# Optimization experiments

Measured on AMD Instinct MI355X. Metric: run time of the kernel, lower is better.

Reference implementation:

```python
import jax, jax.numpy as jnp
import numpy as np

H = 19  # input_size == hidden_size

def setup_inputs() -> dict:
    key = jax.random.key(0)
    ks = jax.random.split(key, 7)
    seq_len, batch = 2048, 1024
    s = 1.0 / np.sqrt(H)  # PyTorch default uniform(-1/sqrt(H), 1/sqrt(H))
    x = jax.random.normal(ks[0], (seq_len, batch, H), dtype=jnp.float32)
    W_ih = jax.random.uniform(ks[1], (3 * H, H), jnp.float32, -s, s)
    W_hh = jax.random.uniform(ks[2], (3 * H, H), jnp.float32, -s, s)
    b_ih = jax.random.uniform(ks[3], (3 * H,), jnp.float32, -s, s)
    b_hh = jax.random.uniform(ks[4], (3 * H,), jnp.float32, -s, s)
    W_out = jax.random.uniform(ks[5], (1, H), jnp.float32, -s, s)
    b_out = jax.random.uniform(ks[6], (1,), jnp.float32, -s, s)
    return {"x": x, "W_ih": W_ih, "W_hh": W_hh, "b_ih": b_ih,
            "b_hh": b_hh, "W_out": W_out, "b_out": b_out}

def _gru(x, W_ih, W_hh, b_ih, b_hh):
    # Precompute all input projections in one big GEMM: [T, B, 3H]
    xg = jnp.einsum('tbi,gi->tbg', x, W_ih) + b_ih
    Whr, Whz, Whn = W_hh[:H], W_hh[H:2*H], W_hh[2*H:]
    bhr, bhz, bhn = b_hh[:H], b_hh[H:2*H], b_hh[2*H:]
    h0 = jnp.zeros(x.shape[1:2] + (H,), dtype=x.dtype)

    def step(h, xg_t):
        xr, xz, xn = xg_t[:, :H], xg_t[:, H:2*H], xg_t[:, 2*H:]
        r = jax.nn.sigmoid(xr + h @ Whr.T + bhr)
        z = jax.nn.sigmoid(xz + h @ Whz.T + bhz)
        n = jnp.tanh(xn + r * (h @ Whn.T + bhn))
        h_new = (1.0 - z) * n + z * h
        return h_new, h_new

    _, r_out = jax.lax.scan(step, h0, xg)  # r_out: [T, B, H]
    return r_out

def reference(x, W_ih, W_hh, b_ih, b_hh, W_out, b_out):
    r_out = _gru(x, W_ih, W_hh, b_ih, b_hh)
    return r_out @ W_out.T + b_out  # [T, B, 1]
```

## Files before the change

kernel.cpp:

```cpp
#include <hip/hip_runtime.h>
#include <math.h>

#define HH 19
#define NG 57
#define SL 64
#define NB 1024
#define TT 2048

typedef float v2f __attribute__((ext_vector_type(2)));
typedef unsigned u2 __attribute__((ext_vector_type(2)));
typedef unsigned u32x4 __attribute__((ext_vector_type(4)));
typedef unsigned u32x2 __attribute__((ext_vector_type(2)));
typedef _Float16 v2h __attribute__((ext_vector_type(2)));

__device__ __forceinline__ float rlf(float v, int l) {
  return __uint_as_float(__builtin_amdgcn_readlane(__float_as_uint(v), l));
}
__device__ __forceinline__ float frcp(float v) { return __builtin_amdgcn_rcpf(v); }
__device__ __forceinline__ float fexp2(float v) {
#if __has_builtin(__builtin_amdgcn_exp2f)
  return __builtin_amdgcn_exp2f(v);
#else
  return exp2f(v);
#endif
}
__device__ __forceinline__ unsigned short f2h(float f) {
  return __builtin_bit_cast(unsigned short, (_Float16)f);
}
__device__ __forceinline__ float h2f(unsigned short u) {
  return (float)__builtin_bit_cast(_Float16, u);
}
__device__ __forceinline__ v2f mk2(float a, float b) { v2f r; r.x = a; r.y = b; return r; }
__device__ __forceinline__ v2f vfma(v2f a, v2f b, v2f c) {
#if __has_builtin(__builtin_elementwise_fma)
  return __builtin_elementwise_fma(a, b, c);
#else
  v2f r; r.x = fmaf(a.x, b.x, c.x); r.y = fmaf(a.y, b.y, c.y); return r;
#endif
}

#if __has_builtin(__builtin_amdgcn_fdot2)
__device__ __forceinline__ float dot2h(v2h w, unsigned d, float acc) {
  return __builtin_amdgcn_fdot2(w, __builtin_bit_cast(v2h, d), acc, false);
}
#else
__device__ __forceinline__ float dot2h(v2h w, unsigned d, float acc) {
  const float fl = h2f((unsigned short)(d & 0xffffu));
  const float fh = h2f((unsigned short)(d >> 16));
  return fmaf((float)w.x, fl, fmaf((float)w.y, fh, acc));
}
#endif

#if __has_builtin(__builtin_amdgcn_permlane32_swap)
#define HAVE_PLS 1
__device__ __forceinline__ u2 pls(float x) {
  unsigned u = __float_as_uint(x);
  return __builtin_amdgcn_permlane32_swap(u, u, false, false);
}
#else
#define HAVE_PLS 0
#endif

__global__ __launch_bounds__(256) void xg_proj4(
    const float* __restrict__ x, const float* __restrict__ Wih,
    const float* __restrict__ bih, const float* __restrict__ bhh,
    unsigned short* __restrict__ xg)
{
  __shared__ __align__(16) float ls[256 * 33];
  const int tid = threadIdx.x;
  const size_t pair0 = (size_t)blockIdx.x * 256;
  const float L2E = 1.4426950408889634f;

  {
    const float* __restrict__ src = x + pair0 * HH;
#pragma unroll
    for (int j = 0; j < HH; ++j) ls[j * 256 + tid] = src[j * 256 + tid];
  }
  __syncthreads();

  float xv[HH];
#pragma unroll
  for (int k = 0; k < HH; ++k) xv[k] = ls[tid * HH + k];
  __syncthreads();

  unsigned short* __restrict__ lsh = (unsigned short*)ls;
#pragma unroll 1
  for (int g = 0; g < NG; ++g) {
    float a = bih[g] + ((g < 2 * HH) ? bhh[g] : 0.0f);
#pragma unroll
    for (int k = 0; k < HH; ++k) a = fmaf(xv[k], Wih[g * HH + k], a);
    a *= (g < 2 * HH) ? -L2E : (2.0f * L2E);
    lsh[tid * 66 + g] = f2h(a);
  }
#pragma unroll
  for (int g = NG; g < SL; ++g) lsh[tid * 66 + g] = 0;
  __syncthreads();

  const unsigned* __restrict__ lsd = (const unsigned*)ls;
  unsigned* __restrict__ xgd = (unsigned*)xg;
#pragma unroll
  for (int i = 0; i < 32; ++i) {
    const int D = tid + i * 256;
    xgd[pair0 * 32 + D] = lsd[(D >> 5) * 33 + (D & 31)];
  }
}

__global__ void __launch_bounds__(64)
__attribute__((amdgpu_waves_per_eu(1, 1)))
gru_rec6(const unsigned short* __restrict__ xg, const float* __restrict__ Whh,
         const float* __restrict__ bhh, const float* __restrict__ Wout,
         const float* __restrict__ bout, float* __restrict__ out)
{
  __shared__ __align__(16) unsigned short hsh16[64];
  const int b = blockIdx.x;
  const int lane = threadIdx.x;
  const float L2E = 1.4426950408889634f;

  int row;
  if (lane < 32)      row = lane;
  else if (lane < 51) row = lane + 6;
  else if (lane < 57) row = lane - 19;
  else                row = 37;
  const bool isn = (row >= 2 * HH);
  const float s = isn ? (2.0f * L2E) : -L2E;

  v2h wh16[10], wo16[10];
#pragma unroll
  for (int j = 0; j < 10; ++j) {
    const int k0 = 2 * j, k1 = 2 * j + 1;
    wh16[j].x = (_Float16)(s * Whh[row * HH + k0]);
    wh16[j].y = (_Float16)((k1 < HH) ? s * Whh[row * HH + k1] : 0.0f);
    wo16[j].x = (_Float16)Wout[k0];
    wo16[j].y = (_Float16)((k1 < HH) ? Wout[k1] : 0.0f);
  }
  const float dinit = isn ? (2.0f * L2E * bhh[row]) : 0.0f;
  const float bo = bout[0];

  const int il = lane < HH ? lane : HH - 1;
  const int zaddr = ((il < 13) ? (19 + il) : (38 + il)) * 4;

#if HAVE_PLS
  bool loIsX;
  {
    unsigned l = (unsigned)lane;
    u2 pr = __builtin_amdgcn_permlane32_swap(l, l, false, false);
    loIsX = ((unsigned)__builtin_amdgcn_readlane((int)pr.x, 32) < 32u);
  }
#define LOBCAST(val, dst) do { u2 _s = pls(val);                        \
    dst = __uint_as_float(loIsX ? _s.x : _s.y); } while (0)
#define HIBCAST(val, dst) do { u2 _s = pls(val);                        \
    dst = __uint_as_float(loIsX ? _s.y : _s.x); } while (0)
#else
  const int loaddr = (lane & 31) * 4;
  const int hiaddr = ((lane & 31) | 32) * 4;
#define LOBCAST(val, dst) dst = __uint_as_float((unsigned)              \
    __builtin_amdgcn_ds_bpermute(loaddr, (int)__float_as_uint(val)))
#define HIBCAST(val, dst) dst = __uint_as_float((unsigned)              \
    __builtin_amdgcn_ds_bpermute(hiaddr, (int)__float_as_uint(val)))
#endif

  float h = 0.0f;

  const unsigned short* __restrict__ xb = xg + (size_t)b * SL + row;
#define LOADX(dst, trow) do { dst = xb[(size_t)(trow) * (NB * SL)]; } while (0)

  unsigned short s0, s1, s2, s3, s4, s5, s6, s7;
  LOADX(s0, 0); LOADX(s1, 1); LOADX(s2, 2); LOADX(s3, 3);
  LOADX(s4, 4); LOADX(s5, 5); LOADX(s6, 6); LOADX(s7, 7);

  u32x4 Pa = {0,0,0,0}, Ra = {0,0,0,0}, Pb, Rb;
  u32x2 Qa = {0,0}, Qb;

#define OPROJ16(Pi, Ri, Qi, ovar) do {                                  \
    float _o0 = bo, _o1 = 0.0f;                                         \
    _o0 = dot2h(wo16[0], Pi.x, _o0); _o1 = dot2h(wo16[1], Pi.y, _o1);   \
    _o0 = dot2h(wo16[2], Pi.z, _o0); _o1 = dot2h(wo16[3], Pi.w, _o1);   \
    _o0 = dot2h(wo16[4], Ri.x, _o0); _o1 = dot2h(wo16[5], Ri.y, _o1);   \
    _o0 = dot2h(wo16[6], Ri.z, _o0); _o1 = dot2h(wo16[7], Ri.w, _o1);   \
    _o0 = dot2h(wo16[8], Qi.x, _o0); _o1 = dot2h(wo16[9], Qi.y, _o1);   \
    ovar = _o0 + _o1;                                                   \
  } while (0)

#define BODY(tcur, slot, Pi, Ri, Qi, Po, Ro, Qo, ovar) do {             \
                       \
    float _a0 = dinit, _a1 = 0.0f;                                      \
    _a0 = dot2h(wh16[0], Pi.x, _a0); _a1 = dot2h(wh16[1], Pi.y, _a1);   \
    _a0 = dot2h(wh16[2], Pi.z, _a0); _a1 = dot2h(wh16[3], Pi.w, _a1);   \
    _a0 = dot2h(wh16[4], Ri.x, _a0); _a1 = dot2h(wh16[5], Ri.y, _a1);   \
    _a0 = dot2h(wh16[6], Ri.z, _a0); _a1 = dot2h(wh16[7], Ri.w, _a1);   \
    _a0 = dot2h(wh16[8], Qi.x, _a0); _a1 = dot2h(wh16[9], Qi.y, _a1);   \
    const float preh = _a0 + _a1;                                       \
    const float xv = h2f(slot);                                         \
    const float pre = xv + preh;                                        \
    const float sig = frcp(fexp2(pre) + 1.0f);                          \
    const int zzi = __builtin_amdgcn_ds_bpermute(                       \
        zaddr, (int)__float_as_uint(sig));                              \
    float rr; LOBCAST(sig, rr);                                         \
    const float arg = fmaf(rr, preh, xv);                               \
    const float nn = fmaf(-2.0f, frcp(fexp2(arg) + 1.0f), 1.0f);        \
    float nh; HIBCAST(nn, nh);                                          \
    const float zz = __uint_as_float((unsigned)zzi);                    \
    h = fmaf(zz, h - nh, nh);                                           \
    \
    hsh16[lane] = f2h(h);                                               \
    Po = *(const u32x4*)&hsh16[0];                                      \
    Ro = *(const u32x4*)&hsh16[8];                                      \
    Qo = *(const u32x2*)&hsh16[16];                                     \
          \
    OPROJ16(Pi, Ri, Qi, ovar);                                          \
    { const int _tl = ((tcur) + 8 < TT) ? (tcur) + 8 : TT - 1;          \
      LOADX(slot, _tl); }                                               \
  } while (0)

  float o0, o1, o2, o3, o4, o5, o6, o7;
  float* __restrict__ ob = out + b;

  for (int t = 0; t < TT; t += 8) {
    BODY(t + 0, s0, Pa, Ra, Qa, Pb, Rb, Qb, o0);
    BODY(t + 1, s1, Pb, Rb, Qb, Pa, Ra, Qa, o1);
    BODY(t + 2, s2, Pa, Ra, Qa, Pb, Rb, Qb, o2);
    BODY(t + 3, s3, Pb, Rb, Qb, Pa, Ra, Qa, o3);
    BODY(t + 4, s4, Pa, Ra, Qa, Pb, Rb, Qb, o4);
    BODY(t + 5, s5, Pb, Rb, Qb, Pa, Ra, Qa, o5);
    BODY(t + 6, s6, Pa, Ra, Qa, Pb, Rb, Qb, o6);
    BODY(t + 7, s7, Pb, Rb, Qb, Pa, Ra, Qa, o7);
    if (lane == 0) {
      ob[(size_t)((t > 0) ? t - 1 : 0) * NB] = o0;
      ob[(size_t)(t + 0) * NB] = o1;
      ob[(size_t)(t + 1) * NB] = o2;
      ob[(size_t)(t + 2) * NB] = o3;
      ob[(size_t)(t + 3) * NB] = o4;
      ob[(size_t)(t + 4) * NB] = o5;
      ob[(size_t)(t + 5) * NB] = o6;
      ob[(size_t)(t + 6) * NB] = o7;
    }
  }

  {
    float oe;
    OPROJ16(Pa, Ra, Qa, oe);
    if (lane == 0) ob[(size_t)(TT - 1) * NB] = oe;
  }

#undef LOADX
#undef BODY
#undef OPROJ16
#undef LOBCAST
#undef HIBCAST
}

__global__ void __launch_bounds__(64)
__attribute__((amdgpu_waves_per_eu(1, 1)))
gru57_v4(const float* __restrict__ x, const float* __restrict__ Wih,
         const float* __restrict__ Whh, const float* __restrict__ bih,
         const float* __restrict__ bhh, const float* __restrict__ Wout,
         const float* __restrict__ bout, float* __restrict__ out)
{
  const int b = blockIdx.x;
  const int lane = threadIdx.x;
  const float L2E = 1.4426950408889634f;

  int row;
  if (lane < 32)      row = lane;
  else if (lane < 51) row = lane + 6;
  else if (lane < 57) row = lane - 19;
  else                row = 37;
  const bool isn = (row >= 2 * HH);
  const float scale = isn ? (2.0f * L2E) : L2E;

  v2f wx2[10], wh2[10], wo2[10];
#pragma unroll
  for (int j = 0; j < 10; ++j) {
    const int k0 = 2 * j, k1 = 2 * j + 1;
    wx2[j].x = Wih[row * HH + k0] * scale;
    wx2[j].y = (k1 < HH) ? Wih[row * HH + k1] * scale : 0.0f;
    wh2[j].x = Whh[row * HH + k0] * scale;
    wh2[j].y = (k1 < HH) ? Whh[row * HH + k1] * scale : 0.0f;
    wo2[j].x = Wout[k0];
    wo2[j].y = (k1 < HH) ? Wout[k1] : 0.0f;
  }
  const float bxv = bih[row] * scale, bhv = bhh[row] * scale;
  const float ax0 = isn ? bxv : (bxv + bhv);
  const float ah0 = isn ? bhv : 0.0f;
  const float bo  = bout[0];

  const int il = lane < HH ? lane : HH - 1;
  const int zaddr = ((il < 13) ? (19 + il) : (38 + il)) * 4;

#if HAVE_PLS
  bool loIsX;
  {
    unsigned l = (unsigned)lane;
    u2 pr = __builtin_amdgcn_permlane32_swap(l, l, false, false);
    loIsX = ((unsigned)__builtin_amdgcn_readlane((int)pr.x, 32) < 32u);
  }
#define LOBCAST(val, dst) do { u2 _s = pls(val);                        \
    dst = __uint_as_float(loIsX ? _s.x : _s.y); } while (0)
#define HIBCAST(val, dst) do { u2 _s = pls(val);                        \
    dst = __uint_as_float(loIsX ? _s.y : _s.x); } while (0)
#else
  const int loaddr = (lane & 31) * 4;
  const int hiaddr = ((lane & 31) | 32) * 4;
#define LOBCAST(val, dst) dst = __uint_as_float((unsigned)              \
    __builtin_amdgcn_ds_bpermute(loaddr, (int)__float_as_uint(val)))
#define HIBCAST(val, dst) dst = __uint_as_float((unsigned)              \
    __builtin_amdgcn_ds_bpermute(hiaddr, (int)__float_as_uint(val)))
#endif

  float h = 0.0f;
  v2f sh2[10];
#pragma unroll
  for (int j = 0; j < 10; ++j) sh2[j] = mk2(0.f, 0.f);

  const int kx = lane < HH ? lane : HH - 1;
  const float* __restrict__ xbase = x + (size_t)b * HH + kx;

#define LOADXF(dst, trow) do { dst = xbase[(size_t)(trow) * (NB * HH)]; } while (0)
#define XBCAST(slot, xu) do {                                           \
    _Pragma("unroll")                                                   \
    for (int _j = 0; _j < 9; ++_j) {                                    \
      xu[_j].x = rlf(slot, 2 * _j);                                     \
      xu[_j].y = rlf(slot, 2 * _j + 1);                                 \
    }                                                                   \
    xu[9].x = rlf(slot, 18); xu[9].y = 0.0f;                            \
  } while (0)
#define XDOT(xu, dstvar) do {                                           \
    v2f _aA = mk2(ax0, 0.0f), _aB = mk2(0.0f, 0.0f);                    \
    _Pragma("unroll")                                                   \
    for (int _j = 0; _j < 5; ++_j)  _aA = vfma(xu[_j], wx2[_j], _aA);   \
    _Pragma("unroll")                                                   \
    for (int _j = 5; _j < 10; ++_j) _aB = vfma(xu[_j], wx2[_j], _aB);   \
    const v2f _s = _aA + _aB;                                           \
    dstvar = _s.x + _s.y;                                               \
  } while (0)

  float xlA, xlB, xlC, xlD;
  LOADXF(xlA, 0); LOADXF(xlB, 1); LOADXF(xlC, 2); LOADXF(xlD, 3);
  float prex;
  { v2f xu0[10]; XBCAST(xlA, xu0); XDOT(xu0, prex); }

#define BODYF(tcur, nslot, lslot) do {                                  \
    v2f ahA = mk2(ah0, 0.0f), ahB = mk2(0.0f, 0.0f);                    \
    _Pragma("unroll")                                                   \
    for (int _j = 0; _j < 5; ++_j)  ahA = vfma(sh2[_j], wh2[_j], ahA);  \
    _Pragma("unroll")                                                   \
    for (int _j = 5; _j < 10; ++_j) ahB = vfma(sh2[_j], wh2[_j], ahB);  \
    float prexN;                                                        \
    { v2f _xu[10]; XBCAST(nslot, _xu); XDOT(_xu, prexN); }              \
    { const int _tl = ((tcur) + 4 < TT) ? (tcur) + 4 : TT - 1;          \
      LOADXF(lslot, _tl); }                                             \
    const v2f ahv = ahA + ahB;                                          \
    const float preh = ahv.x + ahv.y;                                   \
    const float pre  = prex + preh;                                     \
    const float sig  = frcp(1.0f + fexp2(-pre));                        \
    const int zzi = __builtin_amdgcn_ds_bpermute(                       \
        zaddr, (int)__float_as_uint(sig));                              \
    float rr; LOBCAST(sig, rr);                                         \
    const float npre = fmaf(rr, preh, prex);                            \
    const float nn = fmaf(-2.0f, frcp(fexp2(npre) + 1.0f), 1.0f);       \
    float nh; HIBCAST(nn, nh);                                          \
    const float zz = __uint_as_float((unsigned)zzi);                    \
    h = fmaf(zz, h - nh, nh);                                           \
    _Pragma("unroll")                                                   \
    for (int _j = 0; _j < 9; ++_j) {                                    \
      sh2[_j].x = rlf(h, 2 * _j);                                       \
      sh2[_j].y = rlf(h, 2 * _j + 1);                                   \
    }                                                                   \
    sh2[9].x = rlf(h, 18); sh2[9].y = 0.0f;                             \
    v2f oA = mk2(bo, 0.0f), oB = mk2(0.0f, 0.0f);                       \
    _Pragma("unroll")                                                   \
    for (int _j = 0; _j < 5; ++_j)  oA = vfma(sh2[_j], wo2[_j], oA);    \
    _Pragma("unroll")                                                   \
    for (int _j = 5; _j < 10; ++_j) oB = vfma(sh2[_j], wo2[_j], oB);    \
    const v2f ov = oA + oB;                                             \
    if (lane == 0) out[(size_t)(tcur) * NB + b] = ov.x + ov.y;          \
    prex = prexN;                                                       \
  } while (0)

  for (int t = 0; t < TT; t += 4) {
    BODYF(t + 0, xlB, xlA);
    BODYF(t + 1, xlC, xlB);
    BODYF(t + 2, xlD, xlC);
    BODYF(t + 3, xlA, xlD);
  }

#undef LOADXF
#undef XBCAST
#undef XDOT
#undef BODYF
#undef LOBCAST
#undef HIBCAST
}

extern "C" void kernel_launch(void* const* d_in, const int* in_sizes, int n_in,
                              void* d_out, int out_size, void* d_ws, size_t ws_size,
                              hipStream_t stream) {
  const float* x    = (const float*)d_in[0];
  const float* Wih  = (const float*)d_in[1];
  const float* Whh  = (const float*)d_in[2];
  const float* bih  = (const float*)d_in[3];
  const float* bhh  = (const float*)d_in[4];
  const float* Wout = (const float*)d_in[5];
  const float* bout = (const float*)d_in[6];
  float* out = (float*)d_out;

  const size_t need = (size_t)TT * NB * SL * sizeof(unsigned short);
  if (ws_size >= need) {
    unsigned short* xgws = (unsigned short*)d_ws;
    xg_proj4<<<dim3((TT * NB) / 256), dim3(256), 0, stream>>>(
        x, Wih, bih, bhh, xgws);
    gru_rec6<<<dim3(NB), dim3(64), 0, stream>>>(
        xgws, Whh, bhh, Wout, bout, out);
  } else {
    gru57_v4<<<dim3(NB), dim3(64), 0, stream>>>(
        x, Wih, Whh, bih, bhh, Wout, bout, out);
  }
}
```

Measured before the change: 545.1 us.

## Compute z gate redundantly per lane to drop one cross-lane permute from chain

Each lane now evaluates two gate rows: the low half does r plus z, and the high half does n plus z. Previously z had to be fetched with a ds_bpermute from another lane. Computing z locally takes that permute off the serial per-timestep dependency chain. In exchange each step does twice the dot2 work and twice the x loads, and it needs an extra HIBCAST of z and more registers.

```diff
diff --git a/kernel.cpp b/kernel.cpp
--- a/kernel.cpp
+++ b/kernel.cpp
@@ -107,7 +107,7 @@
 
 __global__ void __launch_bounds__(64)
 __attribute__((amdgpu_waves_per_eu(1, 1)))
-gru_rec6(const unsigned short* __restrict__ xg, const float* __restrict__ Whh,
+gru_rec7(const unsigned short* __restrict__ xg, const float* __restrict__ Whh,
          const float* __restrict__ bhh, const float* __restrict__ Wout,
          const float* __restrict__ bout, float* __restrict__ out)
 {
@@ -116,28 +116,25 @@
   const int lane = threadIdx.x;
   const float L2E = 1.4426950408889634f;
 
-  int row;
-  if (lane < 32)      row = lane;
-  else if (lane < 51) row = lane + 6;
-  else if (lane < 57) row = lane - 19;
-  else                row = 37;
-  const bool isn = (row >= 2 * HH);
-  const float s = isn ? (2.0f * L2E) : -L2E;
-
-  v2h wh16[10], wo16[10];
+  const int i19 = (lane & 31) < HH ? (lane & 31) : HH - 1;
+  const bool up = lane >= 32;
+  const int rowA = up ? (2 * HH + i19) : i19;
+  const int rowB = HH + i19;
+  const float sA = up ? (2.0f * L2E) : -L2E;
+
+  v2h wA16[10], wB16[10], wo16[10];
 #pragma unroll
   for (int j = 0; j < 10; ++j) {
     const int k0 = 2 * j, k1 = 2 * j + 1;
-    wh16[j].x = (_Float16)(s * Whh[row * HH + k0]);
-    wh16[j].y = (_Float16)((k1 < HH) ? s * Whh[row * HH + k1] : 0.0f);
+    wA16[j].x = (_Float16)(sA * Whh[rowA * HH + k0]);
+    wA16[j].y = (_Float16)((k1 < HH) ? sA * Whh[rowA * HH + k1] : 0.0f);
+    wB16[j].x = (_Float16)(-L2E * Whh[rowB * HH + k0]);
+    wB16[j].y = (_Float16)((k1 < HH) ? -L2E * Whh[rowB * HH + k1] : 0.0f);
     wo16[j].x = (_Float16)Wout[k0];
     wo16[j].y = (_Float16)((k1 < HH) ? Wout[k1] : 0.0f);
   }
-  const float dinit = isn ? (2.0f * L2E * bhh[row]) : 0.0f;
+  const float dinitA = up ? (2.0f * L2E * bhh[rowA]) : 0.0f;
   const float bo = bout[0];
-
-  const int il = lane < HH ? lane : HH - 1;
-  const int zaddr = ((il < 13) ? (19 + il) : (38 + il)) * 4;
 
 #if HAVE_PLS
   bool loIsX;
@@ -161,12 +158,16 @@
 
   float h = 0.0f;
 
-  const unsigned short* __restrict__ xb = xg + (size_t)b * SL + row;
-#define LOADX(dst, trow) do { dst = xb[(size_t)(trow) * (NB * SL)]; } while (0)
-
-  unsigned short s0, s1, s2, s3, s4, s5, s6, s7;
-  LOADX(s0, 0); LOADX(s1, 1); LOADX(s2, 2); LOADX(s3, 3);
-  LOADX(s4, 4); LOADX(s5, 5); LOADX(s6, 6); LOADX(s7, 7);
+  const unsigned short* __restrict__ xbA = xg + (size_t)b * SL + rowA;
+  const unsigned short* __restrict__ xbB = xg + (size_t)b * SL + rowB;
+#define LOADA(dst, t) do { dst = xbA[(size_t)(t) * (NB * SL)]; } while (0)
+#define LOADB(dst, t) do { dst = xbB[(size_t)(t) * (NB * SL)]; } while (0)
+
+  unsigned short a0,a1,a2,a3,a4,a5,a6,a7, b0,b1,b2,b3,b4,b5,b6,b7;
+  LOADA(a0,0); LOADB(b0,0); LOADA(a1,1); LOADB(b1,1);
+  LOADA(a2,2); LOADB(b2,2); LOADA(a3,3); LOADB(b3,3);
+  LOADA(a4,4); LOADB(b4,4); LOADA(a5,5); LOADB(b5,5);
+  LOADA(a6,6); LOADB(b6,6); LOADA(a7,7); LOADB(b7,7);
 
   u32x4 Pa = {0,0,0,0}, Ra = {0,0,0,0}, Pb, Rb;
   u32x2 Qa = {0,0}, Qb;
@@ -181,49 +182,55 @@
     ovar = _o0 + _o1;                                                   \
   } while (0)
 
-#define BODY(tcur, slot, Pi, Ri, Qi, Po, Ro, Qo, ovar) do {             \
-                       \
-    float _a0 = dinit, _a1 = 0.0f;                                      \
-    _a0 = dot2h(wh16[0], Pi.x, _a0); _a1 = dot2h(wh16[1], Pi.y, _a1);   \
-    _a0 = dot2h(wh16[2], Pi.z, _a0); _a1 = dot2h(wh16[3], Pi.w, _a1);   \
-    _a0 = dot2h(wh16[4], Ri.x, _a0); _a1 = dot2h(wh16[5], Ri.y, _a1);   \
-    _a0 = dot2h(wh16[6], Ri.z, _a0); _a1 = dot2h(wh16[7], Ri.w, _a1);   \
-    _a0 = dot2h(wh16[8], Qi.x, _a0); _a1 = dot2h(wh16[9], Qi.y, _a1);   \
-    const float preh = _a0 + _a1;                                       \
-    const float xv = h2f(slot);                                         \
-    const float pre = xv + preh;                                        \
-    const float sig = frcp(fexp2(pre) + 1.0f);                          \
-    const int zzi = __builtin_amdgcn_ds_bpermute(                       \
-        zaddr, (int)__float_as_uint(sig));                              \
-    float rr; LOBCAST(sig, rr);                                         \
-    const float arg = fmaf(rr, preh, xv);                               \
-    const float nn = fmaf(-2.0f, frcp(fexp2(arg) + 1.0f), 1.0f);        \
-    float nh; HIBCAST(nn, nh);                                          \
-    const float zz = __uint_as_float((unsigned)zzi);                    \
-    h = fmaf(zz, h - nh, nh);                                           \
-    \
+#define BODY(tcur, sa, sb, Pi, Ri, Qi, Po, Ro, Qo, ovar) do {           \
+              \
+    float _a0 = dinitA, _a1 = 0.0f;                                     \
+    _a0 = dot2h(wA16[0], Pi.x, _a0); _a1 = dot2h(wA16[1], Pi.y, _a1);   \
+    _a0 = dot2h(wA16[2], Pi.z, _a0); _a1 = dot2h(wA16[3], Pi.w, _a1);   \
+    _a0 = dot2h(wA16[4], Ri.x, _a0); _a1 = dot2h(wA16[5], Ri.y, _a1);   \
+    _a0 = dot2h(wA16[6], Ri.z, _a0); _a1 = dot2h(wA16[7], Ri.w, _a1);   \
+    _a0 = dot2h(wA16[8], Qi.x, _a0); _a1 = dot2h(wA16[9], Qi.y, _a1);   \
+    const float xvB = h2f(sb);                                          \
+    float _b0 = xvB, _b1 = 0.0f;                                        \
+    _b0 = dot2h(wB16[0], Pi.x, _b0); _b1 = dot2h(wB16[1], Pi.y, _b1);   \
+    _b0 = dot2h(wB16[2], Pi.z, _b0); _b1 = dot2h(wB16[3], Pi.w, _b1);   \
+    _b0 = dot2h(wB16[4], Ri.x, _b0); _b1 = dot2h(wB16[5], Ri.y, _b1);   \
+    _b0 = dot2h(wB16[6], Ri.z, _b0); _b1 = dot2h(wB16[7], Ri.w, _b1);   \
+    _b0 = dot2h(wB16[8], Qi.x, _b0); _b1 = dot2h(wB16[9], Qi.y, _b1);   \
+    const float preA = _a0 + _a1;            \
+    const float xvA = h2f(sa);                                          \
+    const float sigA = frcp(fexp2(xvA + preA) + 1.0f);   \
+    float rr; LOBCAST(sigA, rr);                    \
+    const float preB = _b0 + _b1;                                       \
+    const float zzN = frcp(fexp2(preB) + 1.0f);      \
+    const float arg = fmaf(rr, preA, xvA);                              \
+    const float nnN = fmaf(-2.0f, frcp(fexp2(arg) + 1.0f), 1.0f);       \
+    float nh; HIBCAST(nnN, nh);                     \
+    float zh; HIBCAST(zzN, zh);                     \
+    h = fmaf(zh, h - nh, nh);                                           \
+       \
     hsh16[lane] = f2h(h);                                               \
     Po = *(const u32x4*)&hsh16[0];                                      \
     Ro = *(const u32x4*)&hsh16[8];                                      \
     Qo = *(const u32x2*)&hsh16[16];                                     \
-          \
+            \
     OPROJ16(Pi, Ri, Qi, ovar);                                          \
     { const int _tl = ((tcur) + 8 < TT) ? (tcur) + 8 : TT - 1;          \
-      LOADX(slot, _tl); }                                               \
+      LOADA(sa, _tl); LOADB(sb, _tl); }                                 \
   } while (0)
 
   float o0, o1, o2, o3, o4, o5, o6, o7;
   float* __restrict__ ob = out + b;
 
   for (int t = 0; t < TT; t += 8) {
-    BODY(t + 0, s0, Pa, Ra, Qa, Pb, Rb, Qb, o0);
-    BODY(t + 1, s1, Pb, Rb, Qb, Pa, Ra, Qa, o1);
-    BODY(t + 2, s2, Pa, Ra, Qa, Pb, Rb, Qb, o2);
-    BODY(t + 3, s3, Pb, Rb, Qb, Pa, Ra, Qa, o3);
-    BODY(t + 4, s4, Pa, Ra, Qa, Pb, Rb, Qb, o4);
-    BODY(t + 5, s5, Pb, Rb, Qb, Pa, Ra, Qa, o5);
-    BODY(t + 6, s6, Pa, Ra, Qa, Pb, Rb, Qb, o6);
-    BODY(t + 7, s7, Pb, Rb, Qb, Pa, Ra, Qa, o7);
+    BODY(t + 0, a0, b0, Pa, Ra, Qa, Pb, Rb, Qb, o0);
+    BODY(t + 1, a1, b1, Pb, Rb, Qb, Pa, Ra, Qa, o1);
+    BODY(t + 2, a2, b2, Pa, Ra, Qa, Pb, Rb, Qb, o2);
+    BODY(t + 3, a3, b3, Pb, Rb, Qb, Pa, Ra, Qa, o3);
+    BODY(t + 4, a4, b4, Pa, Ra, Qa, Pb, Rb, Qb, o4);
+    BODY(t + 5, a5, b5, Pb, Rb, Qb, Pa, Ra, Qa, o5);
+    BODY(t + 6, a6, b6, Pa, Ra, Qa, Pb, Rb, Qb, o6);
+    BODY(t + 7, a7, b7, Pb, Rb, Qb, Pa, Ra, Qa, o7);
     if (lane == 0) {
       ob[(size_t)((t > 0) ? t - 1 : 0) * NB] = o0;
       ob[(size_t)(t + 0) * NB] = o1;
@@ -242,7 +249,8 @@
     if (lane == 0) ob[(size_t)(TT - 1) * NB] = oe;
   }
 
-#undef LOADX
+#undef LOADA
+#undef LOADB
 #undef BODY
 #undef OPROJ16
 #undef LOBCAST
@@ -409,7 +417,7 @@
     unsigned short* xgws = (unsigned short*)d_ws;
     xg_proj4<<<dim3((TT * NB) / 256), dim3(256), 0, stream>>>(
         x, Wih, bih, bhh, xgws);
-    gru_rec6<<<dim3(NB), dim3(64), 0, stream>>>(
+    gru_rec7<<<dim3(NB), dim3(64), 0, stream>>>(
         xgws, Whh, bhh, Wout, bout, out);
   } else {
     gru57_v4<<<dim3(NB), dim3(64), 0, stream>>>(
```

Result: slower. 583.8 us (+7.1%).

## Fold output projection into idle lane 57 and prepack scaled input weights

Applied to the files above, without the earlier changes.

The recurrence kernel drops the separate per-step output dot product and makes lane 57, which previously duplicated row 37, compute the W_out projection with the same HDOT path as the gate rows, so it costs no extra instructions. A new tiny wpack kernel pre-scales W_ih and the folded biases into a padded 20-wide layout. The input projection kernel then uses packed two-wide FMAs over these weights instead of scalar FMAs with per-gate scaling. This adds one small kernel launch and a little workspace in exchange for fewer instructions on the recurrence critical path and in the projection kernel.

```diff
diff --git a/kernel.cpp b/kernel.cpp
--- a/kernel.cpp
+++ b/kernel.cpp
@@ -61,15 +61,27 @@
 #define HAVE_PLS 0
 #endif
 
-__global__ __launch_bounds__(256) void xg_proj4(
-    const float* __restrict__ x, const float* __restrict__ Wih,
-    const float* __restrict__ bih, const float* __restrict__ bhh,
+__global__ __launch_bounds__(64) void wpack(
+    const float* __restrict__ Wih, const float* __restrict__ bih,
+    const float* __restrict__ bhh, float* __restrict__ wp)
+{
+  const int t = threadIdx.x + blockIdx.x * 64;
+  if (t < NG * 20) {
+    const int g = t / 20, k = t - g * 20;
+    const float L2E = 1.4426950408889634f;
+    const float s = (g < 2 * HH) ? -L2E : 2.0f * L2E;
+    wp[t] = (k < HH) ? Wih[g * HH + k] * s
+                     : (bih[g] + (g < 2 * HH ? bhh[g] : 0.0f)) * s;
+  }
+}
+
+__global__ __launch_bounds__(256) void xg_proj5(
+    const float* __restrict__ x, const float* __restrict__ wp,
     unsigned short* __restrict__ xg)
 {
   __shared__ __align__(16) float ls[256 * 33];
   const int tid = threadIdx.x;
   const size_t pair0 = (size_t)blockIdx.x * 256;
-  const float L2E = 1.4426950408889634f;
 
   {
     const float* __restrict__ src = x + pair0 * HH;
@@ -78,19 +90,24 @@
   }
   __syncthreads();
 
-  float xv[HH];
-#pragma unroll
-  for (int k = 0; k < HH; ++k) xv[k] = ls[tid * HH + k];
+  v2f xv2[10];
+#pragma unroll
+  for (int j = 0; j < 9; ++j)
+    xv2[j] = mk2(ls[tid * HH + 2 * j], ls[tid * HH + 2 * j + 1]);
+  xv2[9] = mk2(ls[tid * HH + 18], 0.0f);
   __syncthreads();
 
   unsigned short* __restrict__ lsh = (unsigned short*)ls;
 #pragma unroll 1
   for (int g = 0; g < NG; ++g) {
-    float a = bih[g] + ((g < 2 * HH) ? bhh[g] : 0.0f);
-#pragma unroll
-    for (int k = 0; k < HH; ++k) a = fmaf(xv[k], Wih[g * HH + k], a);
-    a *= (g < 2 * HH) ? -L2E : (2.0f * L2E);
-    lsh[tid * 66 + g] = f2h(a);
+    const v2f* __restrict__ wr = (const v2f*)(wp + g * 20);
+    v2f a0 = mk2(wp[g * 20 + HH], 0.0f), a1 = mk2(0.0f, 0.0f);
+#pragma unroll
+    for (int j = 0; j < 5; ++j)  a0 = vfma(xv2[j], wr[j], a0);
+#pragma unroll
+    for (int j = 5; j < 10; ++j) a1 = vfma(xv2[j], wr[j], a1);
+    const v2f sv = a0 + a1;
+    lsh[tid * 66 + g] = f2h(sv.x + sv.y);
   }
 #pragma unroll
   for (int g = NG; g < SL; ++g) lsh[tid * 66 + g] = 0;
@@ -107,7 +124,7 @@
 
 __global__ void __launch_bounds__(64)
 __attribute__((amdgpu_waves_per_eu(1, 1)))
-gru_rec6(const unsigned short* __restrict__ xg, const float* __restrict__ Whh,
+gru_rec8(const unsigned short* __restrict__ xg, const float* __restrict__ Whh,
          const float* __restrict__ bhh, const float* __restrict__ Wout,
          const float* __restrict__ bout, float* __restrict__ out)
 {
@@ -122,19 +139,19 @@
   else if (lane < 57) row = lane - 19;
   else                row = 37;
   const bool isn = (row >= 2 * HH);
+  const bool isO = (lane == 57);
   const float s = isn ? (2.0f * L2E) : -L2E;
 
-  v2h wh16[10], wo16[10];
+  v2h wh16[10];
 #pragma unroll
   for (int j = 0; j < 10; ++j) {
     const int k0 = 2 * j, k1 = 2 * j + 1;
-    wh16[j].x = (_Float16)(s * Whh[row * HH + k0]);
-    wh16[j].y = (_Float16)((k1 < HH) ? s * Whh[row * HH + k1] : 0.0f);
-    wo16[j].x = (_Float16)Wout[k0];
-    wo16[j].y = (_Float16)((k1 < HH) ? Wout[k1] : 0.0f);
-  }
-  const float dinit = isn ? (2.0f * L2E * bhh[row]) : 0.0f;
-  const float bo = bout[0];
+    const float w0 = isO ? Wout[k0] : s * Whh[row * HH + k0];
+    const float w1 = (k1 < HH) ? (isO ? Wout[k1] : s * Whh[row * HH + k1]) : 0.0f;
+    wh16[j].x = (_Float16)w0;
+    wh16[j].y = (_Float16)w1;
+  }
+  const float dinit = isO ? bout[0] : (isn ? (2.0f * L2E * bhh[row]) : 0.0f);
 
   const int il = lane < HH ? lane : HH - 1;
   const int zaddr = ((il < 13) ? (19 + il) : (38 + il)) * 4;
@@ -171,25 +188,19 @@
   u32x4 Pa = {0,0,0,0}, Ra = {0,0,0,0}, Pb, Rb;
   u32x2 Qa = {0,0}, Qb;
 
-#define OPROJ16(Pi, Ri, Qi, ovar) do {                                  \
-    float _o0 = bo, _o1 = 0.0f;                                         \
-    _o0 = dot2h(wo16[0], Pi.x, _o0); _o1 = dot2h(wo16[1], Pi.y, _o1);   \
-    _o0 = dot2h(wo16[2], Pi.z, _o0); _o1 = dot2h(wo16[3], Pi.w, _o1);   \
-    _o0 = dot2h(wo16[4], Ri.x, _o0); _o1 = dot2h(wo16[5], Ri.y, _o1);   \
-    _o0 = dot2h(wo16[6], Ri.z, _o0); _o1 = dot2h(wo16[7], Ri.w, _o1);   \
-    _o0 = dot2h(wo16[8], Qi.x, _o0); _o1 = dot2h(wo16[9], Qi.y, _o1);   \
-    ovar = _o0 + _o1;                                                   \
-  } while (0)
-
-#define BODY(tcur, slot, Pi, Ri, Qi, Po, Ro, Qo, ovar) do {             \
-                       \
+#define HDOT(Pi, Ri, Qi, dstvar) do {                                   \
     float _a0 = dinit, _a1 = 0.0f;                                      \
     _a0 = dot2h(wh16[0], Pi.x, _a0); _a1 = dot2h(wh16[1], Pi.y, _a1);   \
     _a0 = dot2h(wh16[2], Pi.z, _a0); _a1 = dot2h(wh16[3], Pi.w, _a1);   \
     _a0 = dot2h(wh16[4], Ri.x, _a0); _a1 = dot2h(wh16[5], Ri.y, _a1);   \
     _a0 = dot2h(wh16[6], Ri.z, _a0); _a1 = dot2h(wh16[7], Ri.w, _a1);   \
     _a0 = dot2h(wh16[8], Qi.x, _a0); _a1 = dot2h(wh16[9], Qi.y, _a1);   \
-    const float preh = _a0 + _a1;                                       \
+    dstvar = _a0 + _a1;                                                 \
+  } while (0)
+
+#define BODY(tcur, slot, Pi, Ri, Qi, Po, Ro, Qo, ovar) do {             \
+    float preh; HDOT(Pi, Ri, Qi, preh);                                 \
+    ovar = preh;                  \
     const float xv = h2f(slot);                                         \
     const float pre = xv + preh;                                        \
     const float sig = frcp(fexp2(pre) + 1.0f);                          \
@@ -201,13 +212,10 @@
     float nh; HIBCAST(nn, nh);                                          \
     const float zz = __uint_as_float((unsigned)zzi);                    \
     h = fmaf(zz, h - nh, nh);                                           \
-    \
     hsh16[lane] = f2h(h);                                               \
     Po = *(const u32x4*)&hsh16[0];                                      \
     Ro = *(const u32x4*)&hsh16[8];                                      \
     Qo = *(const u32x2*)&hsh16[16];                                     \
-          \
-    OPROJ16(Pi, Ri, Qi, ovar);                                          \
     { const int _tl = ((tcur) + 8 < TT) ? (tcur) + 8 : TT - 1;          \
       LOADX(slot, _tl); }                                               \
   } while (0)
@@ -224,7 +232,7 @@
     BODY(t + 5, s5, Pb, Rb, Qb, Pa, Ra, Qa, o5);
     BODY(t + 6, s6, Pa, Ra, Qa, Pb, Rb, Qb, o6);
     BODY(t + 7, s7, Pb, Rb, Qb, Pa, Ra, Qa, o7);
-    if (lane == 0) {
+    if (lane == 57) {
       ob[(size_t)((t > 0) ? t - 1 : 0) * NB] = o0;
       ob[(size_t)(t + 0) * NB] = o1;
       ob[(size_t)(t + 1) * NB] = o2;
@@ -237,14 +245,13 @@
   }
 
   {
-    float oe;
-    OPROJ16(Pa, Ra, Qa, oe);
-    if (lane == 0) ob[(size_t)(TT - 1) * NB] = oe;
+    float oe; HDOT(Pa, Ra, Qa, oe);
+    if (lane == 57) ob[(size_t)(TT - 1) * NB] = oe;
   }
 
 #undef LOADX
 #undef BODY
-#undef OPROJ16
+#undef HDOT
 #undef LOBCAST
 #undef HIBCAST
 }
@@ -404,12 +411,16 @@
   const float* bout = (const float*)d_in[6];
   float* out = (float*)d_out;
 
-  const size_t need = (size_t)TT * NB * SL * sizeof(unsigned short);
-  if (ws_size >= need) {
+  const size_t xg_bytes = (size_t)TT * NB * SL * sizeof(unsigned short);
+  const size_t wp_bytes = (size_t)NG * 20 * sizeof(float);
+  if (ws_size >= xg_bytes + wp_bytes) {
     unsigned short* xgws = (unsigned short*)d_ws;
-    xg_proj4<<<dim3((TT * NB) / 256), dim3(256), 0, stream>>>(
-        x, Wih, bih, bhh, xgws);
-    gru_rec6<<<dim3(NB), dim3(64), 0, stream>>>(
+    float* wpws = (float*)((char*)d_ws + xg_bytes);
+    wpack<<<dim3((NG * 20 + 63) / 64), dim3(64), 0, stream>>>(
+        Wih, bih, bhh, wpws);
+    xg_proj5<<<dim3((TT * NB) / 256), dim3(256), 0, stream>>>(
+        x, wpws, xgws);
+    gru_rec8<<<dim3(NB), dim3(64), 0, stream>>>(
         xgws, Whh, bhh, Wout, bout, out);
   } else {
     gru57_v4<<<dim3(NB), dim3(64), 0, stream>>>(
```

Measured after the change: 524.8 us. 1.04x faster.
